# Performance work log

Measured on AMD Instinct MI355X. Metric: run time of the kernel, lower is better.

Reference implementation:

```python
import jax, jax.numpy as jnp
import numpy as np

DIM, EMBED, HEADS = 768, 512, 8
HEAD_DIM = EMBED // HEADS


def setup_inputs() -> dict:
    key = jax.random.key(0)
    ks = jax.random.split(key, 11)
    B, S = 4, 2048
    s = 0.02
    return {
        "query": jax.random.normal(ks[0], (B, S, DIM), jnp.float32),
        "key": jax.random.normal(ks[1], (B, S, DIM), jnp.float32),
        "value": jax.random.normal(ks[2], (B, S, DIM), jnp.float32),
        "wq": jax.random.normal(ks[3], (DIM, EMBED), jnp.float32) * s,
        "bq": jnp.zeros((EMBED,), jnp.float32),
        "wk": jax.random.normal(ks[4], (DIM, EMBED), jnp.float32) * s,
        "bk": jnp.zeros((EMBED,), jnp.float32),
        "wv": jax.random.normal(ks[5], (DIM, EMBED), jnp.float32) * s,
        "bv": jnp.zeros((EMBED,), jnp.float32),
        "wo": jax.random.normal(ks[6], (EMBED, DIM), jnp.float32) * s,
        "bo": jnp.zeros((DIM,), jnp.float32),
    }


def reference(query, key, value, wq, bq, wk, bk, wv, bv, wo, bo):
    B, S, _ = query.shape
    # QKV projections -> [B, H, S, Dh]
    def split_heads(x):
        return x.reshape(B, -1, HEADS, HEAD_DIM).transpose(0, 2, 1, 3)
    q = split_heads(query @ wq + bq)
    k = split_heads(key @ wk + bk)
    v = split_heads(value @ wv + bv)
    scores = jnp.einsum("bhqd,bhkd->bhqk", q, k) / jnp.sqrt(jnp.float32(HEAD_DIM))
    p = jax.nn.softmax(scores, axis=-1)
    x = jnp.einsum("bhqk,bhkd->bhqd", p, v)
    x = x.transpose(0, 2, 1, 3).reshape(B, S, EMBED)
    return x @ wo + bo
```

## Files before the change

### kernel.cpp

```cpp
#include <hip/hip_runtime.h>
#include <math.h>

#define NH   8
#define HD   64
#define BS   4
#define SEQL 2048
#define DIMX 768
#define EMB  512
#define MROWS (BS*SEQL)
#define NSPLIT 2
#define KSPAN (SEQL/NSPLIT)

typedef __attribute__((ext_vector_type(4))) float          f32x4;
typedef __attribute__((ext_vector_type(8))) __bf16         bf16x8;
typedef __attribute__((ext_vector_type(8))) unsigned short u16x8;
typedef __attribute__((ext_vector_type(4))) unsigned short u16x4;

union BF8 { u16x8 u; bf16x8 b; };

__device__ __forceinline__ unsigned short f2bf(float x) {
    unsigned int u = __float_as_uint(x);
    u += 0x7FFFu + ((u >> 16) & 1u);
    return (unsigned short)(u >> 16);
}

#if __has_builtin(__builtin_amdgcn_exp2f)
#define EXP2F(x) __builtin_amdgcn_exp2f(x)
#else
#define EXP2F(x) exp2f(x)
#endif

__device__ __forceinline__ bf16x8 ldb8(const unsigned short* p) {
    return *(const bf16x8*)p;
}

__device__ __forceinline__ void gload16(const unsigned short* g, unsigned short* l) {
    __builtin_amdgcn_global_load_lds(
        (const __attribute__((address_space(1))) unsigned int*)(const void*)g,
        (__attribute__((address_space(3))) unsigned int*)(void*)l,
        16, 0, 0);
}

__global__ __launch_bounds__(256)
void cast3(const float* __restrict__ q, const float* __restrict__ k,
           const float* __restrict__ v, unsigned short* __restrict__ out)
{
    const float* src = blockIdx.y == 0 ? q : (blockIdx.y == 1 ? k : v);
    unsigned short* dst = out + (size_t)blockIdx.y * (MROWS * DIMX);
    const int n4 = MROWS * DIMX / 4;
    for (int i = blockIdx.x * 256 + threadIdx.x; i < n4; i += gridDim.x * 256) {
        f32x4 x = ((const f32x4*)src)[i];
        u16x4 o;
        o[0] = f2bf(x[0]); o[1] = f2bf(x[1]); o[2] = f2bf(x[2]); o[3] = f2bf(x[3]);
        ((u16x4*)dst)[i] = o;
    }
}

__global__ __launch_bounds__(256)
void transpose_w4(const float* __restrict__ w0, const float* __restrict__ w1,
                  const float* __restrict__ w2, const float* __restrict__ w3,
                  unsigned short* __restrict__ o0, unsigned short* __restrict__ o1,
                  unsigned short* __restrict__ o2, unsigned short* __restrict__ o3)
{
    __shared__ float sm[32][33];
    const int which = blockIdx.y;
    const float* in; unsigned short* out; int R, C;
    if      (which == 0) { in = w0; out = o0; R = DIMX; C = EMB;  }
    else if (which == 1) { in = w1; out = o1; R = DIMX; C = EMB;  }
    else if (which == 2) { in = w2; out = o2; R = DIMX; C = EMB;  }
    else                 { in = w3; out = o3; R = EMB;  C = DIMX; }
    const int nbx = C / 32;
    const int rB = (blockIdx.x / nbx) * 32, cB = (blockIdx.x % nbx) * 32;
    const int row = threadIdx.x >> 3, c4 = (threadIdx.x & 7) * 4;
    f32x4 v = *(const f32x4*)&in[(size_t)(rB + row) * C + cB + c4];
    sm[row][c4 + 0] = v[0]; sm[row][c4 + 1] = v[1];
    sm[row][c4 + 2] = v[2]; sm[row][c4 + 3] = v[3];
    __syncthreads();
    u16x4 o;
    o[0] = f2bf(sm[c4 + 0][row]); o[1] = f2bf(sm[c4 + 1][row]);
    o[2] = f2bf(sm[c4 + 2][row]); o[3] = f2bf(sm[c4 + 3][row]);
    *(u16x4*)&out[(size_t)(cB + row) * R + rB + c4] = o;
}

template<bool DIRECT>
__device__ __forceinline__ void gemm_core(
    const unsigned short* __restrict__ A, const unsigned short* __restrict__ Bt,
    int K, int mBase, int nBase,
    unsigned short* __restrict__ smA, unsigned short* __restrict__ smB,
    f32x4 (&acc)[4][4])
{
    const int tid = threadIdx.x;
    const int lane = tid & 63, w = tid >> 6;
    const int quad = lane >> 4, lanem = lane & 15;
    const int wm = w >> 1, wn = w & 1;
    const int r8 = lane >> 3, ch = lane & 7;
    const int swz = ((ch ^ r8) << 3);

    const f32x4 z4 = {0.f, 0.f, 0.f, 0.f};
    #pragma unroll
    for (int i = 0; i < 4; ++i)
        #pragma unroll
        for (int j = 0; j < 4; ++j) acc[i][j] = z4;

    const int fxor = (lanem & 7);

    for (int k0 = 0; k0 < K; k0 += 64) {
        __syncthreads();
        #pragma unroll
        for (int j = 0; j < 4; ++j) {
            const int row = (w * 4 + j) * 8 + r8;
            gload16(&A[(size_t)(mBase + row) * K + k0 + swz], smA + (w * 4 + j) * 512);
            gload16(&Bt[(size_t)(nBase + row) * K + k0 + swz], smB + (w * 4 + j) * 512);
        }
        __syncthreads();
        #pragma unroll
        for (int kk = 0; kk < 64; kk += 32) {
            const int cb = kk >> 3;
            bf16x8 xa[4], wb[4];
            #pragma unroll
            for (int mt = 0; mt < 4; ++mt)
                xa[mt] = ldb8(&smA[(wm * 64 + mt * 16 + lanem) * 64 + (((cb + quad) ^ fxor) << 3)]);
            #pragma unroll
            for (int nt = 0; nt < 4; ++nt)
                wb[nt] = ldb8(&smB[(wn * 64 + nt * 16 + lanem) * 64 + (((cb + quad) ^ fxor) << 3)]);
            if constexpr (DIRECT) {
                #pragma unroll
                for (int mt = 0; mt < 4; ++mt)
                    #pragma unroll
                    for (int nt = 0; nt < 4; ++nt)
                        acc[mt][nt] = __builtin_amdgcn_mfma_f32_16x16x32_bf16(xa[mt], wb[nt], acc[mt][nt], 0, 0, 0);
            } else {
                #pragma unroll
                for (int nt = 0; nt < 4; ++nt)
                    #pragma unroll
                    for (int mt = 0; mt < 4; ++mt)
                        acc[nt][mt] = __builtin_amdgcn_mfma_f32_16x16x32_bf16(wb[nt], xa[mt], acc[nt][mt], 0, 0, 0);
            }
        }
    }
}

__global__ __launch_bounds__(256)
void gemm_qkv(const unsigned short* __restrict__ Xc, const unsigned short* __restrict__ Wt,
              const float* __restrict__ bq, const float* __restrict__ bk,
              const float* __restrict__ bv,
              unsigned short* __restrict__ Qb, unsigned short* __restrict__ Kb,
              unsigned short* __restrict__ Vtb)
{
    __shared__ unsigned short smA[128 * 64];
    __shared__ unsigned short smB[128 * 64];
    const int z = blockIdx.z;
    const unsigned short* A  = Xc + (size_t)z * (MROWS * DIMX);
    const unsigned short* Bt = Wt + (size_t)z * (EMB * DIMX);
    const float* bias = z == 0 ? bq : (z == 1 ? bk : bv);
    const int mBase = blockIdx.y * 128, nBase = blockIdx.x * 128;

    const int tid = threadIdx.x;
    const int lane = tid & 63, w = tid >> 6;
    const int quad = lane >> 4, lanem = lane & 15;
    const int wm = w >> 1, wn = w & 1;

    f32x4 acc[4][4];
    if (z == 2) {
        gemm_core<true>(A, Bt, DIMX, mBase, nBase, smA, smB, acc);
        #pragma unroll
        for (int mt = 0; mt < 4; ++mt) {
            const int sg = mBase + wm * 64 + mt * 16 + quad * 4;
            const int b = sg >> 11, s = sg & 2047;
            #pragma unroll
            for (int nt = 0; nt < 4; ++nt) {
                const int de = nBase + wn * 64 + nt * 16 + lanem;
                const float bvv = bias[de];
                const int h = de >> 6, dh = de & 63;
                u16x4 ov;
                #pragma unroll
                for (int r = 0; r < 4; ++r) ov[r] = f2bf(acc[mt][nt][r] + bvv);
                *(u16x4*)&Vtb[((size_t)((b * NH + h) * HD + dh) << 11) + s] = ov;
            }
        }
    } else {
        gemm_core<false>(A, Bt, DIMX, mBase, nBase, smA, smB, acc);
        const float os = (z == 0) ? 0.18033688f : 1.0f;
        unsigned short* C = (z == 0) ? Qb : Kb;
        #pragma unroll
        for (int nt = 0; nt < 4; ++nt) {
            const int n0 = nBase + wn * 64 + nt * 16 + quad * 4;
            const f32x4 b4 = *(const f32x4*)&bias[n0];
            #pragma unroll
            for (int mt = 0; mt < 4; ++mt) {
                const int m = mBase + wm * 64 + mt * 16 + lanem;
                u16x4 ov;
                #pragma unroll
                for (int r = 0; r < 4; ++r) ov[r] = f2bf((acc[nt][mt][r] + b4[r]) * os);
                *(u16x4*)&C[(size_t)m * EMB + n0] = ov;
            }
        }
    }
}

__global__ __launch_bounds__(256)
void gemm_out(const unsigned short* __restrict__ Xb, const unsigned short* __restrict__ Wot,
              const float* __restrict__ bo, float* __restrict__ out)
{
    __shared__ unsigned short smA[128 * 64];
    __shared__ unsigned short smB[128 * 64];
    const int mBase = blockIdx.y * 128, nBase = blockIdx.x * 128;
    const int tid = threadIdx.x;
    const int lane = tid & 63, w = tid >> 6;
    const int quad = lane >> 4, lanem = lane & 15;
    const int wm = w >> 1, wn = w & 1;

    f32x4 acc[4][4];
    gemm_core<false>(Xb, Wot, EMB, mBase, nBase, smA, smB, acc);
    #pragma unroll
    for (int nt = 0; nt < 4; ++nt) {
        const int n0 = nBase + wn * 64 + nt * 16 + quad * 4;
        const f32x4 b4 = *(const f32x4*)&bo[n0];
        #pragma unroll
        for (int mt = 0; mt < 4; ++mt) {
            const int m = mBase + wm * 64 + mt * 16 + lanem;
            f32x4 ov = acc[nt][mt] + b4;
            *(f32x4*)&out[(size_t)m * DIMX + n0] = ov;
        }
    }
}

__global__ __launch_bounds__(256)
void attn_mfma(const unsigned short* __restrict__ Qb, const unsigned short* __restrict__ Kb,
               const unsigned short* __restrict__ Vt,
               float* __restrict__ Opart, float* __restrict__ lpart)
{
    __shared__ unsigned short smK[64 * 72];
    __shared__ unsigned short smV[64 * 72];
    __shared__ unsigned short smP[4][32 * 72];
    const int id = blockIdx.x;
    const int bh = ((id & 7) << 2) | ((id >> 3) & 3);
    const int rest = id >> 5;
    const int qb = rest & 15, sp = rest >> 4;
    const int b = bh >> 3, h = bh & 7;

    const int tid = threadIdx.x;
    const int w = tid >> 6, lane = tid & 63;
    const int quad = lane >> 4, lanem = lane & 15;

    bf16x8 aq[2][2];
    #pragma unroll
    for (int rg = 0; rg < 2; ++rg) {
        const size_t qrow = (size_t)(b * SEQL + qb * 128 + w * 32 + rg * 16 + lanem) * EMB + h * HD;
        aq[rg][0] = ldb8(&Qb[qrow + quad * 8]);
        aq[rg][1] = ldb8(&Qb[qrow + 32 + quad * 8]);
    }

    const f32x4 z4 = {0.f, 0.f, 0.f, 0.f};
    f32x4 o[4][2];
    f32x4 ls[2] = {z4, z4};
    #pragma unroll
    for (int dt = 0; dt < 4; ++dt)
        #pragma unroll
        for (int rg = 0; rg < 2; ++rg) o[dt][rg] = z4;

    BF8 ones;
    #pragma unroll
    for (int i = 0; i < 8; ++i) ones.u[i] = 0x3F80;

    const unsigned short* Kbase = Kb + (size_t)b * SEQL * EMB + h * HD;
    const unsigned short* Vbase = Vt + (size_t)bh * HD * SEQL;
    unsigned short* pW = &smP[w][0];
    const int srow = tid >> 3, c8 = (tid & 7) * 8;

    for (int t = 0; t < KSPAN / 64; ++t) {
        const int k0 = sp * KSPAN + t * 64;
        u16x8 kv[2], vv[2];
        #pragma unroll
        for (int p = 0; p < 2; ++p) {
            kv[p] = *(const u16x8*)&Kbase[(size_t)(k0 + srow + p * 32) * EMB + c8];
            vv[p] = *(const u16x8*)&Vbase[(size_t)(srow + p * 32) * SEQL + k0 + c8];
        }
        __syncthreads();
        #pragma unroll
        for (int p = 0; p < 2; ++p) {
            *(u16x8*)&smK[(srow + p * 32) * 72 + c8] = kv[p];
            *(u16x8*)&smV[(srow + p * 32) * 72 + c8] = vv[p];
        }
        __syncthreads();

        #pragma unroll
        for (int nt = 0; nt < 4; ++nt) {
            bf16x8 bk0 = ldb8(&smK[(nt * 16 + lanem) * 72 + quad * 8]);
            bf16x8 bk1 = ldb8(&smK[(nt * 16 + lanem) * 72 + 32 + quad * 8]);
            #pragma unroll
            for (int rg = 0; rg < 2; ++rg) {
                f32x4 s = __builtin_amdgcn_mfma_f32_16x16x32_bf16(bk0, aq[rg][0], z4, 0, 0, 0);
                s = __builtin_amdgcn_mfma_f32_16x16x32_bf16(bk1, aq[rg][1], s, 0, 0, 0);
                u16x4 pk;
                #pragma unroll
                for (int r = 0; r < 4; ++r)
                    pk[r] = (unsigned short)(__float_as_uint(EXP2F(s[r])) >> 16);
                *(u16x4*)&pW[(rg * 16 + lanem) * 72 + nt * 16 + quad * 4] = pk;
            }
        }
        bf16x8 pb[2][2];
        #pragma unroll
        for (int rg = 0; rg < 2; ++rg) {
            pb[rg][0] = ldb8(&pW[(rg * 16 + lanem) * 72 + quad * 8]);
            pb[rg][1] = ldb8(&pW[(rg * 16 + lanem) * 72 + 32 + quad * 8]);
        }
        #pragma unroll
        for (int dt = 0; dt < 4; ++dt) {
            bf16x8 av0 = ldb8(&smV[(dt * 16 + lanem) * 72 + quad * 8]);
            bf16x8 av1 = ldb8(&smV[(dt * 16 + lanem) * 72 + 32 + quad * 8]);
            #pragma unroll
            for (int rg = 0; rg < 2; ++rg) {
                o[dt][rg] = __builtin_amdgcn_mfma_f32_16x16x32_bf16(av0, pb[rg][0], o[dt][rg], 0, 0, 0);
                o[dt][rg] = __builtin_amdgcn_mfma_f32_16x16x32_bf16(av1, pb[rg][1], o[dt][rg], 0, 0, 0);
            }
        }
        #pragma unroll
        for (int rg = 0; rg < 2; ++rg) {
            ls[rg] = __builtin_amdgcn_mfma_f32_16x16x32_bf16(ones.b, pb[rg][0], ls[rg], 0, 0, 0);
            ls[rg] = __builtin_amdgcn_mfma_f32_16x16x32_bf16(ones.b, pb[rg][1], ls[rg], 0, 0, 0);
        }
    }

    #pragma unroll
    for (int rg = 0; rg < 2; ++rg) {
        const int qloc = qb * 128 + w * 32 + rg * 16 + lanem;
        float* orow = Opart + ((size_t)sp * 32 * SEQL + (size_t)bh * SEQL + qloc) * HD;
        #pragma unroll
        for (int dt = 0; dt < 4; ++dt)
            *(f32x4*)&orow[dt * 16 + quad * 4] = o[dt][rg];
        if (quad == 0)
            lpart[(size_t)sp * 32 * SEQL + (size_t)bh * SEQL + qloc] = ls[rg][0];
    }
}

__global__ __launch_bounds__(256)
void attn_reduce(const float* __restrict__ Opart, const float* __restrict__ lpart,
                 unsigned short* __restrict__ Xb)
{
    const int lin = blockIdx.x * 256 + threadIdx.x;
    const int d4 = (lin & 15) << 2;
    const int q = (lin >> 4) & 2047;
    const int bh = lin >> 15;
    const int b = bh >> 3, h = bh & 7;
    const size_t base = ((size_t)bh * SEQL + q) * HD + d4;
    const size_t soff = (size_t)32 * SEQL * HD;
    f32x4 o0 = *(const f32x4*)&Opart[base];
    f32x4 o1 = *(const f32x4*)&Opart[base + soff];
    const float l0 = lpart[(size_t)bh * SEQL + q];
    const float l1 = lpart[(size_t)32 * SEQL + (size_t)bh * SEQL + q];
    const float rl = 1.f / (l0 + l1);
    u16x4 ov;
    #pragma unroll
    for (int r = 0; r < 4; ++r) ov[r] = f2bf((o0[r] + o1[r]) * rl);
    *(u16x4*)&Xb[((size_t)(b * SEQL + q)) * EMB + h * HD + d4] = ov;
}

extern "C" void kernel_launch(void* const* d_in, const int* in_sizes, int n_in,
                              void* d_out, int out_size, void* d_ws, size_t ws_size,
                              hipStream_t stream) {
    (void)in_sizes; (void)n_in; (void)out_size; (void)ws_size;
    const float* query = (const float*)d_in[0];
    const float* key   = (const float*)d_in[1];
    const float* value = (const float*)d_in[2];
    const float* wq = (const float*)d_in[3];
    const float* bq = (const float*)d_in[4];
    const float* wk = (const float*)d_in[5];
    const float* bk = (const float*)d_in[6];
    const float* wv = (const float*)d_in[7];
    const float* bv = (const float*)d_in[8];
    const float* wo = (const float*)d_in[9];
    const float* bo = (const float*)d_in[10];
    float* out = (float*)d_out;

    char* ws = (char*)d_ws;
    unsigned short* castb = (unsigned short*)(ws);
    float*          Opart = (float*)(ws);
    float*          lpart = (float*)(ws + 33554432);
    unsigned short* Wt    = (unsigned short*)(ws + 37748736);
    unsigned short* Wot   = (unsigned short*)(ws + 40108032);
    unsigned short* Qbuf  = (unsigned short*)(ws + 40894464);
    unsigned short* Xbuf  = Qbuf;
    unsigned short* Kbuf  = (unsigned short*)(ws + 49283072);
    unsigned short* Vtb   = (unsigned short*)(ws + 57671680);

    const dim3 blk(256);

    transpose_w4<<<dim3(384, 4), blk, 0, stream>>>(wq, wk, wv, wo,
        Wt, Wt + (size_t)EMB * DIMX, Wt + 2 * (size_t)EMB * DIMX, Wot);
    cast3<<<dim3(1024, 3), blk, 0, stream>>>(query, key, value, castb);

    gemm_qkv<<<dim3(EMB / 128, MROWS / 128, 3), blk, 0, stream>>>(
        castb, Wt, bq, bk, bv, Qbuf, Kbuf, Vtb);

    attn_mfma<<<dim3(32 * 16 * NSPLIT), blk, 0, stream>>>(Qbuf, Kbuf, Vtb, Opart, lpart);
    attn_reduce<<<dim3(4096), blk, 0, stream>>>(Opart, lpart, Xbuf);

    gemm_out<<<dim3(DIMX / 128, MROWS / 128), blk, 0, stream>>>(Xbuf, Wot, bo, out);
}
```

Baseline: 240.7 us.

## Fuse input cast into QKV GEMM and split-K reduce into output GEMM

Result: slower. 261.5 us (+8.6%).

```diff
diff --git a/kernel.cpp b/kernel.cpp
--- a/kernel.cpp
+++ b/kernel.cpp
@@ -39,21 +39,6 @@
         (const __attribute__((address_space(1))) unsigned int*)(const void*)g,
         (__attribute__((address_space(3))) unsigned int*)(void*)l,
         16, 0, 0);
-}
-
-__global__ __launch_bounds__(256)
-void cast3(const float* __restrict__ q, const float* __restrict__ k,
-           const float* __restrict__ v, unsigned short* __restrict__ out)
-{
-    const float* src = blockIdx.y == 0 ? q : (blockIdx.y == 1 ? k : v);
-    unsigned short* dst = out + (size_t)blockIdx.y * (MROWS * DIMX);
-    const int n4 = MROWS * DIMX / 4;
-    for (int i = blockIdx.x * 256 + threadIdx.x; i < n4; i += gridDim.x * 256) {
-        f32x4 x = ((const f32x4*)src)[i];
-        u16x4 o;
-        o[0] = f2bf(x[0]); o[1] = f2bf(x[1]); o[2] = f2bf(x[2]); o[3] = f2bf(x[3]);
-        ((u16x4*)dst)[i] = o;
-    }
 }
 
 __global__ __launch_bounds__(256)
@@ -82,10 +67,12 @@
     *(u16x4*)&out[(size_t)(cB + row) * R + rB + c4] = o;
 }
 
-template<bool DIRECT>
+template<bool DIRECT, int AMODE>
 __device__ __forceinline__ void gemm_core(
-    const unsigned short* __restrict__ A, const unsigned short* __restrict__ Bt,
-    int K, int mBase, int nBase,
+    const float* __restrict__ A, const float* __restrict__ A2,
+    const float* __restrict__ lp0, const float* __restrict__ lp1,
+    const unsigned short* __restrict__ Bt,
+    int K, int lda, int mBase, int nBase,
     unsigned short* __restrict__ smA, unsigned short* __restrict__ smB,
     f32x4 (&acc)[4][4])
 {
@@ -105,11 +92,39 @@
     const int fxor = (lanem & 7);
 
     for (int k0 = 0; k0 < K; k0 += 64) {
+        u16x8 sa[4];
+        #pragma unroll
+        for (int j = 0; j < 4; ++j) {
+            const int m = mBase + (w * 4 + j) * 8 + r8;
+            const int kc = k0 + swz;
+            if constexpr (AMODE == 1) {
+                const float* ap = &A[(size_t)m * lda + kc];
+                f32x4 x0 = *(const f32x4*)ap;
+                f32x4 x1 = *(const f32x4*)(ap + 4);
+                #pragma unroll
+                for (int r = 0; r < 4; ++r) { sa[j][r] = f2bf(x0[r]); sa[j][4 + r] = f2bf(x1[r]); }
+            } else {
+                const int q = m & 2047, bb = m >> 11, hh = kc >> 6, dd = kc & 63;
+                const size_t off = ((((size_t)((bb << 3) | hh)) * 2048 + q) << 6) + dd;
+                f32x4 a0 = *(const f32x4*)&A [off];
+                f32x4 a1 = *(const f32x4*)&A [off + 4];
+                f32x4 c0 = *(const f32x4*)&A2[off];
+                f32x4 c1 = *(const f32x4*)&A2[off + 4];
+                const float rl = 1.f / (lp0[off >> 6] + lp1[off >> 6]);
+                #pragma unroll
+                for (int r = 0; r < 4; ++r) {
+                    sa[j][r]     = f2bf((a0[r] + c0[r]) * rl);
+                    sa[j][4 + r] = f2bf((a1[r] + c1[r]) * rl);
+                }
+            }
+        }
         __syncthreads();
+        #pragma unroll
+        for (int j = 0; j < 4; ++j)
+            *(u16x8*)&smA[(w * 4 + j) * 512 + lane * 8] = sa[j];
         #pragma unroll
         for (int j = 0; j < 4; ++j) {
             const int row = (w * 4 + j) * 8 + r8;
-            gload16(&A[(size_t)(mBase + row) * K + k0 + swz], smA + (w * 4 + j) * 512);
             gload16(&Bt[(size_t)(nBase + row) * K + k0 + swz], smB + (w * 4 + j) * 512);
         }
         __syncthreads();
@@ -141,7 +156,8 @@
 }
 
 __global__ __launch_bounds__(256)
-void gemm_qkv(const unsigned short* __restrict__ Xc, const unsigned short* __restrict__ Wt,
+void gemm_qkv(const float* __restrict__ Xq, const float* __restrict__ Xk,
+              const float* __restrict__ Xv, const unsigned short* __restrict__ Wt,
               const float* __restrict__ bq, const float* __restrict__ bk,
               const float* __restrict__ bv,
               unsigned short* __restrict__ Qb, unsigned short* __restrict__ Kb,
@@ -150,7 +166,7 @@
     __shared__ unsigned short smA[128 * 64];
     __shared__ unsigned short smB[128 * 64];
     const int z = blockIdx.z;
-    const unsigned short* A  = Xc + (size_t)z * (MROWS * DIMX);
+    const float* A = z == 0 ? Xq : (z == 1 ? Xk : Xv);
     const unsigned short* Bt = Wt + (size_t)z * (EMB * DIMX);
     const float* bias = z == 0 ? bq : (z == 1 ? bk : bv);
     const int mBase = blockIdx.y * 128, nBase = blockIdx.x * 128;
@@ -162,7 +178,7 @@
 
     f32x4 acc[4][4];
     if (z == 2) {
-        gemm_core<true>(A, Bt, DIMX, mBase, nBase, smA, smB, acc);
+        gemm_core<true, 1>(A, nullptr, nullptr, nullptr, Bt, DIMX, DIMX, mBase, nBase, smA, smB, acc);
         #pragma unroll
         for (int mt = 0; mt < 4; ++mt) {
             const int sg = mBase + wm * 64 + mt * 16 + quad * 4;
@@ -179,7 +195,7 @@
             }
         }
     } else {
-        gemm_core<false>(A, Bt, DIMX, mBase, nBase, smA, smB, acc);
+        gemm_core<false, 1>(A, nullptr, nullptr, nullptr, Bt, DIMX, DIMX, mBase, nBase, smA, smB, acc);
         const float os = (z == 0) ? 0.18033688f : 1.0f;
         unsigned short* C = (z == 0) ? Qb : Kb;
         #pragma unroll
@@ -199,7 +215,8 @@
 }
 
 __global__ __launch_bounds__(256)
-void gemm_out(const unsigned short* __restrict__ Xb, const unsigned short* __restrict__ Wot,
+void gemm_out(const float* __restrict__ Opart, const float* __restrict__ lpart,
+              const unsigned short* __restrict__ Wot,
               const float* __restrict__ bo, float* __restrict__ out)
 {
     __shared__ unsigned short smA[128 * 64];
@@ -210,8 +227,11 @@
     const int quad = lane >> 4, lanem = lane & 15;
     const int wm = w >> 1, wn = w & 1;
 
+    const float* Op1 = Opart + (size_t)32 * SEQL * HD;
+    const float* lp1 = lpart + (size_t)32 * SEQL;
+
     f32x4 acc[4][4];
-    gemm_core<false>(Xb, Wot, EMB, mBase, nBase, smA, smB, acc);
+    gemm_core<false, 2>(Opart, Op1, lpart, lp1, Wot, EMB, EMB, mBase, nBase, smA, smB, acc);
     #pragma unroll
     for (int nt = 0; nt < 4; ++nt) {
         const int n0 = nBase + wn * 64 + nt * 16 + quad * 4;
@@ -332,28 +352,6 @@
         if (quad == 0)
             lpart[(size_t)sp * 32 * SEQL + (size_t)bh * SEQL + qloc] = ls[rg][0];
     }
-}
-
-__global__ __launch_bounds__(256)
-void attn_reduce(const float* __restrict__ Opart, const float* __restrict__ lpart,
-                 unsigned short* __restrict__ Xb)
-{
-    const int lin = blockIdx.x * 256 + threadIdx.x;
-    const int d4 = (lin & 15) << 2;
-    const int q = (lin >> 4) & 2047;
-    const int bh = lin >> 15;
-    const int b = bh >> 3, h = bh & 7;
-    const size_t base = ((size_t)bh * SEQL + q) * HD + d4;
-    const size_t soff = (size_t)32 * SEQL * HD;
-    f32x4 o0 = *(const f32x4*)&Opart[base];
-    f32x4 o1 = *(const f32x4*)&Opart[base + soff];
-    const float l0 = lpart[(size_t)bh * SEQL + q];
-    const float l1 = lpart[(size_t)32 * SEQL + (size_t)bh * SEQL + q];
-    const float rl = 1.f / (l0 + l1);
-    u16x4 ov;
-    #pragma unroll
-    for (int r = 0; r < 4; ++r) ov[r] = f2bf((o0[r] + o1[r]) * rl);
-    *(u16x4*)&Xb[((size_t)(b * SEQL + q)) * EMB + h * HD + d4] = ov;
 }
 
 extern "C" void kernel_launch(void* const* d_in, const int* in_sizes, int n_in,
@@ -374,13 +372,11 @@
     float* out = (float*)d_out;
 
     char* ws = (char*)d_ws;
-    unsigned short* castb = (unsigned short*)(ws);
     float*          Opart = (float*)(ws);
     float*          lpart = (float*)(ws + 33554432);
     unsigned short* Wt    = (unsigned short*)(ws + 37748736);
     unsigned short* Wot   = (unsigned short*)(ws + 40108032);
     unsigned short* Qbuf  = (unsigned short*)(ws + 40894464);
-    unsigned short* Xbuf  = Qbuf;
     unsigned short* Kbuf  = (unsigned short*)(ws + 49283072);
     unsigned short* Vtb   = (unsigned short*)(ws + 57671680);
 
@@ -388,13 +384,11 @@
 
     transpose_w4<<<dim3(384, 4), blk, 0, stream>>>(wq, wk, wv, wo,
         Wt, Wt + (size_t)EMB * DIMX, Wt + 2 * (size_t)EMB * DIMX, Wot);
-    cast3<<<dim3(1024, 3), blk, 0, stream>>>(query, key, value, castb);
 
     gemm_qkv<<<dim3(EMB / 128, MROWS / 128, 3), blk, 0, stream>>>(
-        castb, Wt, bq, bk, bv, Qbuf, Kbuf, Vtb);
+        query, key, value, Wt, bq, bk, bv, Qbuf, Kbuf, Vtb);
 
     attn_mfma<<<dim3(32 * 16 * NSPLIT), blk, 0, stream>>>(Qbuf, Kbuf, Vtb, Opart, lpart);
-    attn_reduce<<<dim3(4096), blk, 0, stream>>>(Opart, lpart, Xbuf);
-
-    gemm_out<<<dim3(DIMX / 128, MROWS / 128), blk, 0, stream>>>(Xbuf, Wot, bo, out);
-}
+
+    gemm_out<<<dim3(DIMX / 128, MROWS / 128), blk, 0, stream>>>(Opart, lpart, Wot, bo, out);
+}
```
